# Optimization experiments

Hardware: AMD Instinct MI355X
Metric: run time of the kernel (lower is better)

Reference implementation:

```python
import jax, jax.numpy as jnp
import numpy as np

N = 125000   # lattice cells (50^3)
K = 26       # max neighbors (3D Moore neighborhood)
D = 32       # state_size
STEPS = 3    # CNF integration steps (explicit Euler)


def setup_inputs() -> dict:
    key = jax.random.key(0)
    ks = jax.random.split(key, 12)
    s = 0.1  # small init so tanh stays in its linear-ish regime
    return {
        "full_lattice_states": jax.random.normal(ks[0], (N, D), jnp.float32),
        "neighbor_indices": jax.random.randint(ks[1], (N, K), 0, N, jnp.int32),
        "tier_ids": jax.random.randint(ks[2], (N, K), 0, 3, jnp.int32),
        # local expert (SimpleLinear): [cur ; local_agg] -> D
        "W_loc": jax.random.normal(ks[3], (2 * D, D), jnp.float32) * s,
        "b_loc": jnp.zeros((D,), jnp.float32),
        # functional expert (HybridGNN): per-neighbor message + combine
        "W_msg": jax.random.normal(ks[4], (D, D), jnp.float32) * s,
        "b_msg": jnp.zeros((D,), jnp.float32),
        "W_fun": jax.random.normal(ks[5], (2 * D, D), jnp.float32) * s,
        "b_fun": jnp.zeros((D,), jnp.float32),
        # distant expert (LightweightCNF): ODE drift on [x ; distant_agg]
        "W_cnf": jax.random.normal(ks[6], (2 * D, D), jnp.float32) * s,
        "b_cnf": jnp.zeros((D,), jnp.float32),
        # gating network: [cur ; local_agg ; func_agg ; dist_agg] -> 3 experts
        "W_gate": jax.random.normal(ks[7], (4 * D, 3), jnp.float32) * s,
        "b_gate": jnp.zeros((3,), jnp.float32),
    }


def reference(full_lattice_states, neighbor_indices, tier_ids,
              W_loc, b_loc, W_msg, b_msg, W_fun, b_fun,
              W_cnf, b_cnf, W_gate, b_gate):
    cur = full_lattice_states                      # [N, D]
    nbr = full_lattice_states[neighbor_indices]    # [N, K, D] gather (irregular access)

    def tier_mean(x, t):
        # masked mean over neighbors belonging to tier t
        m = (tier_ids == t)[..., None].astype(x.dtype)           # [N, K, 1]
        return (x * m).sum(axis=1) / jnp.maximum(m.sum(axis=1), 1.0)  # [N, D]

    local_agg = tier_mean(nbr, 0)   # [N, D]
    func_agg = tier_mean(nbr, 1)    # [N, D]
    dist_agg = tier_mean(nbr, 2)    # [N, D]

    # local expert: single linear on [cur ; local_agg]
    local_out = jnp.tanh(jnp.concatenate([cur, local_agg], -1) @ W_loc + b_loc)

    # functional expert: GNN message passing over functional-tier neighbors
    msgs = jnp.tanh(nbr @ W_msg + b_msg)           # [N, K, D]
    func_msg = tier_mean(msgs, 1)                  # [N, D]
    func_out = jnp.tanh(jnp.concatenate([cur, func_msg], -1) @ W_fun + b_fun)

    # distant expert: lightweight CNF, explicit Euler conditioned on dist_agg
    dt = 1.0 / STEPS
    x = cur
    for _ in range(STEPS):
        x = x + dt * jnp.tanh(jnp.concatenate([x, dist_agg], -1) @ W_cnf + b_cnf)
    dist_out = x

    # gating: adaptive weighting of the 3 experts
    gate_in = jnp.concatenate([cur, local_agg, func_agg, dist_agg], -1)  # [N, 4D]
    w = jax.nn.softmax(gate_in @ W_gate + b_gate, axis=-1)               # [N, 3]

    out = (w[:, 0:1] * local_out + w[:, 1:2] * func_out + w[:, 2:3] * dist_out)
    return out
```

## Files before the change

kernel.cpp:

```cpp
#include <hip/hip_runtime.h>
#include <hip/hip_bf16.h>
#include <math.h>

#define NCELL 125000
#define KNBR  26
#define D     32

__device__ __forceinline__ float fast_tanh(float x) {
    float e = __expf(2.0f * x);
    return 1.0f - 2.0f / (e + 1.0f);
}

__global__ void __launch_bounds__(256) msg_kernel(
    const float* __restrict__ X, const float* __restrict__ Wm,
    const float* __restrict__ bm,
    __hip_bfloat16* __restrict__ Mh, __hip_bfloat16* __restrict__ Xh)
{
    __shared__ float sX[256];
    int t = blockIdx.x * 256 + threadIdx.x;
    float v = X[t];
    sX[threadIdx.x] = v;
    Xh[t] = __float2bfloat16(v);
    __syncthreads();
    int d = t & 31;
    int base = threadIdx.x & ~31;
    float acc = bm[d];
#pragma unroll
    for (int j = 0; j < D; ++j)
        acc = fmaf(sX[base + j], Wm[j * D + d], acc);
    Mh[t] = __float2bfloat16(fast_tanh(acc));
}

__global__ void __launch_bounds__(256) agg_kernel(
    const __hip_bfloat16* __restrict__ Xh, const __hip_bfloat16* __restrict__ Mh,
    const int* __restrict__ nbr, const int* __restrict__ tier,
    float* __restrict__ aggs)
{
    __shared__ int sPack[8 * KNBR];
    int tid = threadIdx.x;
    int blockCell = blockIdx.x * 8;
    if (tid < 8 * KNBR) {
        int g = blockCell * KNBR + tid;
        sPack[tid] = (nbr[g] << 2) | tier[g];
    }
    __syncthreads();

    int grp = tid >> 5, d = tid & 31;
    int c = blockCell + grp;
    float sAll = 0.f, s0 = 0.f, s1 = 0.f, sm = 0.f;
    int n0 = 0, n1 = 0;
#pragma unroll
    for (int k = 0; k < KNBR; ++k) {
        int pk = sPack[grp * KNBR + k];
        int tt = pk & 3;
        int j  = pk >> 2;
        float x = __bfloat162float(Xh[j * D + d]);
        bool t0 = (tt == 0), t1 = (tt == 1);
        sAll += x;
        s0 += t0 ? x : 0.f;  n0 += t0;
        s1 += t1 ? x : 0.f;  n1 += t1;
        if (t1) sm += __bfloat162float(Mh[j * D + d]);
    }
    float s2 = sAll - s0 - s1;
    float n2 = (float)(KNBR - n0 - n1);
    float la = s0 / fmaxf((float)n0, 1.f);
    float fa = s1 / fmaxf((float)n1, 1.f);
    float da = s2 / fmaxf(n2, 1.f);
    float fm = sm / fmaxf((float)n1, 1.f);
    float* a = aggs + (size_t)c * 4 * D + d;
    a[0 * D] = la;
    a[1 * D] = fa;
    a[2 * D] = da;
    a[3 * D] = fm;
}

__device__ __forceinline__ void matvec32(const float* __restrict__ in,
                                         const float* __restrict__ W,
                                         float acc[D])
{
#pragma unroll 8
    for (int j = 0; j < D; ++j) {
        float v = in[j];
#pragma unroll
        for (int d = 0; d < D; ++d)
            acc[d] = fmaf(v, W[j * D + d], acc[d]);
    }
}

__global__ void __launch_bounds__(256) expert_kernel(
    const float* __restrict__ X, const float* __restrict__ aggs,
    const float* __restrict__ Wl, const float* __restrict__ bl,
    const float* __restrict__ Wf, const float* __restrict__ bf,
    const float* __restrict__ Wc, const float* __restrict__ bc,
    const float* __restrict__ Wg, const float* __restrict__ bg,
    __hip_bfloat16* __restrict__ pl, __hip_bfloat16* __restrict__ pf,
    float* __restrict__ wgt, float* __restrict__ out)
{
    int c = blockIdx.x * 256 + threadIdx.x;
    if (c >= NCELL) return;
    const float* xr = X    + (size_t)c * D;
    const float* ar = aggs + (size_t)c * 4 * D;
    int e = blockIdx.y;

    if (e == 0) {
        float acc[D];
#pragma unroll
        for (int d = 0; d < D; ++d) acc[d] = bl[d];
        matvec32(xr, Wl, acc);
        matvec32(ar, Wl + D * D, acc);
#pragma unroll
        for (int d = 0; d < D; ++d)
            pl[(size_t)c * D + d] = __float2bfloat16(fast_tanh(acc[d]));
    } else if (e == 1) {
        float acc[D];
#pragma unroll
        for (int d = 0; d < D; ++d) acc[d] = bf[d];
        matvec32(xr, Wf, acc);
        matvec32(ar + 3 * D, Wf + D * D, acc);
#pragma unroll
        for (int d = 0; d < D; ++d)
            pf[(size_t)c * D + d] = __float2bfloat16(fast_tanh(acc[d]));
    } else if (e == 2) {
        float gc[D];
#pragma unroll
        for (int d = 0; d < D; ++d) gc[d] = bc[d];
        matvec32(ar + 2 * D, Wc + D * D, gc);
        float xx[D];
#pragma unroll
        for (int d = 0; d < D; ++d) xx[d] = xr[d];
        const float dt = 1.0f / 3.0f;
#pragma unroll 1
        for (int s = 0; s < 3; ++s) {
            float a2[D];
#pragma unroll
            for (int d = 0; d < D; ++d) a2[d] = gc[d];
#pragma unroll 8
            for (int j = 0; j < D; ++j) {
                float v = xx[j];
#pragma unroll
                for (int d = 0; d < D; ++d)
                    a2[d] = fmaf(v, Wc[j * D + d], a2[d]);
            }
#pragma unroll
            for (int d = 0; d < D; ++d)
                xx[d] += dt * fast_tanh(a2[d]);
        }
#pragma unroll
        for (int d = 0; d < D; ++d) out[(size_t)c * D + d] = xx[d];
    } else {
        float g0 = bg[0], g1 = bg[1], g2 = bg[2];
        const float* ins[4] = { xr, ar, ar + D, ar + 2 * D };
#pragma unroll
        for (int b = 0; b < 4; ++b) {
            const float* in = ins[b];
#pragma unroll 8
            for (int j = 0; j < D; ++j) {
                float v = in[j];
                g0 = fmaf(v, Wg[(b * D + j) * 3 + 0], g0);
                g1 = fmaf(v, Wg[(b * D + j) * 3 + 1], g1);
                g2 = fmaf(v, Wg[(b * D + j) * 3 + 2], g2);
            }
        }
        float mx = fmaxf(g0, fmaxf(g1, g2));
        float e0 = __expf(g0 - mx), e1 = __expf(g1 - mx), e2 = __expf(g2 - mx);
        float inv = 1.f / (e0 + e1 + e2);
        float4 w = make_float4(e0 * inv, e1 * inv, e2 * inv, 0.f);
        *(float4*)(wgt + (size_t)c * 4) = w;
    }
}

__global__ void __launch_bounds__(256) combine_kernel(
    const __hip_bfloat16* __restrict__ pl, const __hip_bfloat16* __restrict__ pf,
    const float* __restrict__ wgt, float* __restrict__ out)
{
    int t = blockIdx.x * 256 + threadIdx.x;
    int c = t >> 5;
    float w0 = wgt[c * 4 + 0], w1 = wgt[c * 4 + 1], w2 = wgt[c * 4 + 2];
    out[t] = w0 * __bfloat162float(pl[t]) + w1 * __bfloat162float(pf[t]) + w2 * out[t];
}

extern "C" void kernel_launch(void* const* d_in, const int* in_sizes, int n_in,
                              void* d_out, int out_size, void* d_ws, size_t ws_size,
                              hipStream_t stream)
{
    const float* X    = (const float*)d_in[0];
    const int*   nbr  = (const int*)  d_in[1];
    const int*   tier = (const int*)  d_in[2];
    const float* Wl   = (const float*)d_in[3];
    const float* bl   = (const float*)d_in[4];
    const float* Wm   = (const float*)d_in[5];
    const float* bm   = (const float*)d_in[6];
    const float* Wf   = (const float*)d_in[7];
    const float* bf   = (const float*)d_in[8];
    const float* Wc   = (const float*)d_in[9];
    const float* bc   = (const float*)d_in[10];
    const float* Wg   = (const float*)d_in[11];
    const float* bg   = (const float*)d_in[12];
    float* out = (float*)d_out;

    const size_t ND = (size_t)NCELL * D;
    __hip_bfloat16* Mh = (__hip_bfloat16*)d_ws;
    __hip_bfloat16* Xh = Mh + ND;
    __hip_bfloat16* pl = Mh;
    __hip_bfloat16* pf = Xh;
    float* aggs = (float*)(Xh + ND);
    float* wgt  = aggs + (size_t)NCELL * 4 * D;

    dim3 blk(256);
    int ndBlocks = (int)(ND / 256);
    msg_kernel<<<dim3(ndBlocks), blk, 0, stream>>>(X, Wm, bm, Mh, Xh);
    agg_kernel<<<dim3(NCELL / 8), blk, 0, stream>>>(Xh, Mh, nbr, tier, aggs);
    expert_kernel<<<dim3((NCELL + 255) / 256, 4), blk, 0, stream>>>(
        X, aggs, Wl, bl, Wf, bf, Wc, bc, Wg, bg, pl, pf, wgt, out);
    combine_kernel<<<dim3(ndBlocks), blk, 0, stream>>>(pl, pf, wgt, out);
}
```

Measured before the change: 266.6 us.

## Fuse expert, gating and combine kernels into one block-tiled MoE kernel

Replaces the four-way expert kernel and the separate combine kernel with a single kernel. Each block loads 128 cells of X into swizzled shared memory. Half the threads compute gating plus the CNF expert while the other half compute the local and functional experts, and the weighted combine happens in shared memory before a coalesced write. Aggregates are now stored as bf16 and read with vector loads, which reduces intermediate traffic and removes the pl/pf/wgt round trips, at the cost of lower precision and register pressure from several 32-wide arrays per thread.

```diff
diff --git a/kernel.cpp b/kernel.cpp
--- a/kernel.cpp
+++ b/kernel.cpp
@@ -5,10 +5,25 @@
 #define NCELL 125000
 #define KNBR  26
 #define D     32
+#define CB    128
 
 __device__ __forceinline__ float fast_tanh(float x) {
     float e = __expf(2.0f * x);
     return 1.0f - 2.0f / (e + 1.0f);
+}
+__device__ __forceinline__ float bf2f(unsigned int h) {
+    return __uint_as_float(h << 16);
+}
+__device__ __forceinline__ void load_row_bf16(const unsigned short* __restrict__ p,
+                                              float* __restrict__ dst) {
+#pragma unroll
+    for (int k = 0; k < 4; ++k) {
+        uint4 v = *(const uint4*)(p + k * 8);
+        dst[k*8+0] = bf2f(v.x & 0xffff); dst[k*8+1] = bf2f(v.x >> 16);
+        dst[k*8+2] = bf2f(v.y & 0xffff); dst[k*8+3] = bf2f(v.y >> 16);
+        dst[k*8+4] = bf2f(v.z & 0xffff); dst[k*8+5] = bf2f(v.z >> 16);
+        dst[k*8+6] = bf2f(v.w & 0xffff); dst[k*8+7] = bf2f(v.w >> 16);
+    }
 }
 
 __global__ void __launch_bounds__(256) msg_kernel(
@@ -34,7 +49,7 @@
 __global__ void __launch_bounds__(256) agg_kernel(
     const __hip_bfloat16* __restrict__ Xh, const __hip_bfloat16* __restrict__ Mh,
     const int* __restrict__ nbr, const int* __restrict__ tier,
-    float* __restrict__ aggs)
+    __hip_bfloat16* __restrict__ aggs)
 {
     __shared__ int sPack[8 * KNBR];
     int tid = threadIdx.x;
@@ -63,120 +78,184 @@
     }
     float s2 = sAll - s0 - s1;
     float n2 = (float)(KNBR - n0 - n1);
-    float la = s0 / fmaxf((float)n0, 1.f);
-    float fa = s1 / fmaxf((float)n1, 1.f);
-    float da = s2 / fmaxf(n2, 1.f);
-    float fm = sm / fmaxf((float)n1, 1.f);
-    float* a = aggs + (size_t)c * 4 * D + d;
-    a[0 * D] = la;
-    a[1 * D] = fa;
-    a[2 * D] = da;
-    a[3 * D] = fm;
-}
-
-__device__ __forceinline__ void matvec32(const float* __restrict__ in,
-                                         const float* __restrict__ W,
-                                         float acc[D])
-{
-#pragma unroll 8
-    for (int j = 0; j < D; ++j) {
-        float v = in[j];
-#pragma unroll
-        for (int d = 0; d < D; ++d)
-            acc[d] = fmaf(v, W[j * D + d], acc[d]);
-    }
-}
-
-__global__ void __launch_bounds__(256) expert_kernel(
-    const float* __restrict__ X, const float* __restrict__ aggs,
+    __hip_bfloat16* a = aggs + (size_t)c * 4 * D + d;
+    a[0 * D] = __float2bfloat16(s0 / fmaxf((float)n0, 1.f));
+    a[1 * D] = __float2bfloat16(s1 / fmaxf((float)n1, 1.f));
+    a[2 * D] = __float2bfloat16(s2 / fmaxf(n2, 1.f));
+    a[3 * D] = __float2bfloat16(sm / fmaxf((float)n1, 1.f));
+}
+
+__global__ void __launch_bounds__(256) moe_kernel(
+    const float* __restrict__ X, const unsigned short* __restrict__ aggs,
     const float* __restrict__ Wl, const float* __restrict__ bl,
-    const float* __restrict__ Wf, const float* __restrict__ bf,
+    const float* __restrict__ Wf, const float* __restrict__ bfv,
     const float* __restrict__ Wc, const float* __restrict__ bc,
     const float* __restrict__ Wg, const float* __restrict__ bg,
-    __hip_bfloat16* __restrict__ pl, __hip_bfloat16* __restrict__ pf,
-    float* __restrict__ wgt, float* __restrict__ out)
-{
-    int c = blockIdx.x * 256 + threadIdx.x;
-    if (c >= NCELL) return;
-    const float* xr = X    + (size_t)c * D;
-    const float* ar = aggs + (size_t)c * 4 * D;
-    int e = blockIdx.y;
-
-    if (e == 0) {
-        float acc[D];
-#pragma unroll
-        for (int d = 0; d < D; ++d) acc[d] = bl[d];
-        matvec32(xr, Wl, acc);
-        matvec32(ar, Wl + D * D, acc);
-#pragma unroll
-        for (int d = 0; d < D; ++d)
-            pl[(size_t)c * D + d] = __float2bfloat16(fast_tanh(acc[d]));
-    } else if (e == 1) {
-        float acc[D];
-#pragma unroll
-        for (int d = 0; d < D; ++d) acc[d] = bf[d];
-        matvec32(xr, Wf, acc);
-        matvec32(ar + 3 * D, Wf + D * D, acc);
-#pragma unroll
-        for (int d = 0; d < D; ++d)
-            pf[(size_t)c * D + d] = __float2bfloat16(fast_tanh(acc[d]));
-    } else if (e == 2) {
-        float gc[D];
-#pragma unroll
-        for (int d = 0; d < D; ++d) gc[d] = bc[d];
-        matvec32(ar + 2 * D, Wc + D * D, gc);
-        float xx[D];
-#pragma unroll
-        for (int d = 0; d < D; ++d) xx[d] = xr[d];
-        const float dt = 1.0f / 3.0f;
+    float* __restrict__ out)
+{
+    __shared__ float sX[CB * D];
+    __shared__ float sW[CB * 4];
+    int tid  = threadIdx.x;
+    int base = blockIdx.x * CB;
+    int limit = (NCELL - base) * D; if (limit > CB * D) limit = CB * D;
+
+    const float4* gX = (const float4*)(X + (size_t)base * D);
+#pragma unroll
+    for (int k = 0; k < (CB * D / 4) / 256; ++k) {
+        int g = tid + k * 256;
+        if (g * 4 < limit) {
+            float4 v = gX[g];
+            int cc = g >> 3;
+            int j0 = (g & 7) << 2;
+            *(float4*)&sX[cc * D + (j0 ^ ((cc & 7) << 2))] = v;
+        }
+    }
+    __syncthreads();
+
+    int half = tid >> 7;
+    int cc   = tid & 127;
+    int c    = base + cc;
+    bool active = (c < NCELL);
+
+    float cur[D];
+    if (active) {
+#pragma unroll
+        for (int j4 = 0; j4 < 8; ++j4) {
+            float4 v = *(float4*)&sX[cc * D + ((j4 << 2) ^ ((cc & 7) << 2))];
+            cur[j4*4+0] = v.x; cur[j4*4+1] = v.y; cur[j4*4+2] = v.z; cur[j4*4+3] = v.w;
+        }
+    }
+    __syncthreads();
+
+    float lo[D], fo[D];
+    if (active) {
+        const unsigned short* ag = aggs + (size_t)c * 4 * D;
+        if (half == 0) {
+            float g0 = bg[0], g1 = bg[1], g2 = bg[2];
+#pragma unroll 8
+            for (int j = 0; j < D; ++j) {
+                float v = cur[j];
+                g0 = fmaf(v, Wg[j*3+0], g0); g1 = fmaf(v, Wg[j*3+1], g1); g2 = fmaf(v, Wg[j*3+2], g2);
+            }
+            float tmp[D];
+            load_row_bf16(ag + 0 * D, tmp);
+#pragma unroll 8
+            for (int j = 0; j < D; ++j) {
+                float v = tmp[j];
+                g0 = fmaf(v, Wg[(D+j)*3+0], g0); g1 = fmaf(v, Wg[(D+j)*3+1], g1); g2 = fmaf(v, Wg[(D+j)*3+2], g2);
+            }
+            load_row_bf16(ag + 1 * D, tmp);
+#pragma unroll 8
+            for (int j = 0; j < D; ++j) {
+                float v = tmp[j];
+                g0 = fmaf(v, Wg[(2*D+j)*3+0], g0); g1 = fmaf(v, Wg[(2*D+j)*3+1], g1); g2 = fmaf(v, Wg[(2*D+j)*3+2], g2);
+            }
+            float da[D];
+            load_row_bf16(ag + 2 * D, da);
+#pragma unroll 8
+            for (int j = 0; j < D; ++j) {
+                float v = da[j];
+                g0 = fmaf(v, Wg[(3*D+j)*3+0], g0); g1 = fmaf(v, Wg[(3*D+j)*3+1], g1); g2 = fmaf(v, Wg[(3*D+j)*3+2], g2);
+            }
+            float mx = fmaxf(g0, fmaxf(g1, g2));
+            float e0 = __expf(g0 - mx), e1 = __expf(g1 - mx), e2 = __expf(g2 - mx);
+            float inv = 1.f / (e0 + e1 + e2);
+            *(float4*)&sW[cc * 4] = make_float4(e0 * inv, e1 * inv, e2 * inv, 0.f);
+
+            float gc[D];
+#pragma unroll
+            for (int d = 0; d < D; ++d) gc[d] = bc[d];
+#pragma unroll 8
+            for (int j = 0; j < D; ++j) {
+                float v = da[j];
+#pragma unroll
+                for (int d = 0; d < D; ++d) gc[d] = fmaf(v, Wc[(D + j) * D + d], gc[d]);
+            }
+            float xx[D];
+#pragma unroll
+            for (int d = 0; d < D; ++d) xx[d] = cur[d];
+            const float dt = 1.0f / 3.0f;
 #pragma unroll 1
-        for (int s = 0; s < 3; ++s) {
-            float a2[D];
-#pragma unroll
-            for (int d = 0; d < D; ++d) a2[d] = gc[d];
-#pragma unroll 8
-            for (int j = 0; j < D; ++j) {
-                float v = xx[j];
-#pragma unroll
-                for (int d = 0; d < D; ++d)
-                    a2[d] = fmaf(v, Wc[j * D + d], a2[d]);
-            }
-#pragma unroll
-            for (int d = 0; d < D; ++d)
-                xx[d] += dt * fast_tanh(a2[d]);
-        }
-#pragma unroll
-        for (int d = 0; d < D; ++d) out[(size_t)c * D + d] = xx[d];
-    } else {
-        float g0 = bg[0], g1 = bg[1], g2 = bg[2];
-        const float* ins[4] = { xr, ar, ar + D, ar + 2 * D };
-#pragma unroll
-        for (int b = 0; b < 4; ++b) {
-            const float* in = ins[b];
-#pragma unroll 8
-            for (int j = 0; j < D; ++j) {
-                float v = in[j];
-                g0 = fmaf(v, Wg[(b * D + j) * 3 + 0], g0);
-                g1 = fmaf(v, Wg[(b * D + j) * 3 + 1], g1);
-                g2 = fmaf(v, Wg[(b * D + j) * 3 + 2], g2);
-            }
-        }
-        float mx = fmaxf(g0, fmaxf(g1, g2));
-        float e0 = __expf(g0 - mx), e1 = __expf(g1 - mx), e2 = __expf(g2 - mx);
-        float inv = 1.f / (e0 + e1 + e2);
-        float4 w = make_float4(e0 * inv, e1 * inv, e2 * inv, 0.f);
-        *(float4*)(wgt + (size_t)c * 4) = w;
-    }
-}
-
-__global__ void __launch_bounds__(256) combine_kernel(
-    const __hip_bfloat16* __restrict__ pl, const __hip_bfloat16* __restrict__ pf,
-    const float* __restrict__ wgt, float* __restrict__ out)
-{
-    int t = blockIdx.x * 256 + threadIdx.x;
-    int c = t >> 5;
-    float w0 = wgt[c * 4 + 0], w1 = wgt[c * 4 + 1], w2 = wgt[c * 4 + 2];
-    out[t] = w0 * __bfloat162float(pl[t]) + w1 * __bfloat162float(pf[t]) + w2 * out[t];
+            for (int s = 0; s < 3; ++s) {
+                float a2[D];
+#pragma unroll
+                for (int d = 0; d < D; ++d) a2[d] = gc[d];
+#pragma unroll 8
+                for (int j = 0; j < D; ++j) {
+                    float v = xx[j];
+#pragma unroll
+                    for (int d = 0; d < D; ++d) a2[d] = fmaf(v, Wc[j * D + d], a2[d]);
+                }
+#pragma unroll
+                for (int d = 0; d < D; ++d) xx[d] += dt * fast_tanh(a2[d]);
+            }
+#pragma unroll
+            for (int j4 = 0; j4 < 8; ++j4) {
+                float4 v = make_float4(xx[j4*4+0], xx[j4*4+1], xx[j4*4+2], xx[j4*4+3]);
+                *(float4*)&sX[cc * D + ((j4 << 2) ^ ((cc & 7) << 2))] = v;
+            }
+        } else {
+            float accL[D], accF[D];
+#pragma unroll
+            for (int d = 0; d < D; ++d) { accL[d] = bl[d]; accF[d] = bfv[d]; }
+#pragma unroll 8
+            for (int j = 0; j < D; ++j) {
+                float v = cur[j];
+#pragma unroll
+                for (int d = 0; d < D; ++d) {
+                    accL[d] = fmaf(v, Wl[j * D + d], accL[d]);
+                    accF[d] = fmaf(v, Wf[j * D + d], accF[d]);
+                }
+            }
+            float tmp[D];
+            load_row_bf16(ag + 0 * D, tmp);
+#pragma unroll 8
+            for (int j = 0; j < D; ++j) {
+                float v = tmp[j];
+#pragma unroll
+                for (int d = 0; d < D; ++d) accL[d] = fmaf(v, Wl[(D + j) * D + d], accL[d]);
+            }
+            load_row_bf16(ag + 3 * D, tmp);
+#pragma unroll 8
+            for (int j = 0; j < D; ++j) {
+                float v = tmp[j];
+#pragma unroll
+                for (int d = 0; d < D; ++d) accF[d] = fmaf(v, Wf[(D + j) * D + d], accF[d]);
+            }
+#pragma unroll
+            for (int d = 0; d < D; ++d) { lo[d] = fast_tanh(accL[d]); fo[d] = fast_tanh(accF[d]); }
+        }
+    }
+    __syncthreads();
+
+    if (active && half == 1) {
+        float4 wv = *(float4*)&sW[cc * 4];
+        float o[D];
+#pragma unroll
+        for (int j4 = 0; j4 < 8; ++j4) {
+            float4 v = *(float4*)&sX[cc * D + ((j4 << 2) ^ ((cc & 7) << 2))];
+            o[j4*4+0] = wv.x * lo[j4*4+0] + wv.y * fo[j4*4+0] + wv.z * v.x;
+            o[j4*4+1] = wv.x * lo[j4*4+1] + wv.y * fo[j4*4+1] + wv.z * v.y;
+            o[j4*4+2] = wv.x * lo[j4*4+2] + wv.y * fo[j4*4+2] + wv.z * v.z;
+            o[j4*4+3] = wv.x * lo[j4*4+3] + wv.y * fo[j4*4+3] + wv.z * v.w;
+        }
+#pragma unroll
+        for (int j4 = 0; j4 < 8; ++j4)
+            *(float4*)&sX[cc * D + ((j4 << 2) ^ ((cc & 7) << 2))] =
+                make_float4(o[j4*4+0], o[j4*4+1], o[j4*4+2], o[j4*4+3]);
+    }
+    __syncthreads();
+
+    float4* gO = (float4*)(out + (size_t)base * D);
+#pragma unroll
+    for (int k = 0; k < (CB * D / 4) / 256; ++k) {
+        int g = tid + k * 256;
+        if (g * 4 < limit) {
+            int cc2 = g >> 3;
+            int j0  = (g & 7) << 2;
+            gO[g] = *(float4*)&sX[cc2 * D + (j0 ^ ((cc2 & 7) << 2))];
+        }
+    }
 }
 
 extern "C" void kernel_launch(void* const* d_in, const int* in_sizes, int n_in,
@@ -199,18 +278,13 @@
     float* out = (float*)d_out;
 
     const size_t ND = (size_t)NCELL * D;
-    __hip_bfloat16* Mh = (__hip_bfloat16*)d_ws;
-    __hip_bfloat16* Xh = Mh + ND;
-    __hip_bfloat16* pl = Mh;
-    __hip_bfloat16* pf = Xh;
-    float* aggs = (float*)(Xh + ND);
-    float* wgt  = aggs + (size_t)NCELL * 4 * D;
+    __hip_bfloat16* Mh   = (__hip_bfloat16*)d_ws;
+    __hip_bfloat16* Xh   = Mh + ND;
+    __hip_bfloat16* aggs = Xh + ND;
 
     dim3 blk(256);
-    int ndBlocks = (int)(ND / 256);
-    msg_kernel<<<dim3(ndBlocks), blk, 0, stream>>>(X, Wm, bm, Mh, Xh);
+    msg_kernel<<<dim3(ND / 256), blk, 0, stream>>>(X, Wm, bm, Mh, Xh);
     agg_kernel<<<dim3(NCELL / 8), blk, 0, stream>>>(Xh, Mh, nbr, tier, aggs);
-    expert_kernel<<<dim3((NCELL + 255) / 256, 4), blk, 0, stream>>>(
-        X, aggs, Wl, bl, Wf, bf, Wc, bc, Wg, bg, pl, pf, wgt, out);
-    combine_kernel<<<dim3(ndBlocks), blk, 0, stream>>>(pl, pf, wgt, out);
-}
+    moe_kernel<<<dim3((NCELL + CB - 1) / CB), blk, 0, stream>>>(
+        X, (const unsigned short*)aggs, Wl, bl, Wf, bf, Wc, bc, Wg, bg, out);
+}
```

Result: faster. 243.3 us (-8.8%).
